# Kernel tuning notes

Hardware: AMD Instinct MI355X
Metric: run time of the kernel (lower is better)

## Reference

```python
import jax, jax.numpy as jnp
import numpy as np

# LoFTR coarse matching at 640x480 / 8 resolution
N, C = 2, 256
H0, W0, H1, W1 = 60, 80, 60, 80
L, S = H0 * W0, H1 * W1
THR = 0.2          # config['thr']
BORDER = 2         # config['border_rm']
TEMP = 0.1         # config['dsmax_temperature']


def setup_inputs() -> dict:
    key = jax.random.key(0)
    k0, k1 = jax.random.split(key)
    return {
        "feat_c0": jax.random.normal(k0, (N, L, C), dtype=jnp.float32),
        "feat_c1": jax.random.normal(k1, (N, S, C), dtype=jnp.float32),
    }


def _border_ok():
    # interior mask (no 'mask0' in data path): zero out BORDER cells on every side
    def interior(n):
        i = jnp.arange(n)
        return (i >= BORDER) & (i < n - BORDER)
    ok = (interior(H0)[:, None, None, None]
          & interior(W0)[None, :, None, None]
          & interior(H1)[None, None, :, None]
          & interior(W1)[None, None, None, :])  # [H0,W0,H1,W1]
    return ok.reshape(L, S)


def reference(feat_c0, feat_c1):
    # feature normalization by sqrt(C)
    scale = 1.0 / (C ** 0.5)
    f0 = feat_c0 * scale
    f1 = feat_c1 * scale
    # similarity + dual softmax
    sim = jnp.einsum('nlc,nsc->nls', f0, f1) / TEMP           # [N,L,S]
    conf = jax.nn.softmax(sim, axis=1) * jax.nn.softmax(sim, axis=2)
    # threshold + border removal
    mask = (conf > THR) & _border_ok()[None]                  # [N,L,S]
    # mutual nearest neighbour
    mask = mask & (conf == conf.max(axis=2, keepdims=True)) \
                & (conf == conf.max(axis=1, keepdims=True))
    # dense fixed-shape match extraction (equivalent to b_ids/i_ids/j_ids/mconf):
    mask_v = mask.any(axis=2)                                  # [N,L] row has a match
    j_ids = jnp.argmax(mask, axis=2).astype(jnp.int32)         # [N,L] matched column
    mconf = jnp.where(
        mask_v,
        jnp.take_along_axis(conf, j_ids[..., None].astype(jnp.int64), axis=2)[..., 0],
        0.0,
    )                                                          # [N,L]
    return conf, mask_v, j_ids, mconf
```

## Files before the change

kernel.cpp:

```cpp
#include <hip/hip_runtime.h>

#define L 4800
#define S 4800
#define C 256
#define NB 2
#define STRIPS 600
#define THRV 0.2f

typedef _Float16 f16;
typedef _Float16 f16x8 __attribute__((ext_vector_type(8)));
typedef float f32x4 __attribute__((ext_vector_type(4)));

__global__ __launch_bounds__(256) void k_convert(const float* __restrict__ a, const float* __restrict__ b,
                                                 f16* __restrict__ ah, f16* __restrict__ bh) {
    const int PER = NB * L * C / 4;
    int idx = blockIdx.x * 256 + threadIdx.x;
    const float4* src;
    unsigned long long* dst;
    int i;
    if (idx < PER) { src = reinterpret_cast<const float4*>(a); dst = reinterpret_cast<unsigned long long*>(ah); i = idx; }
    else           { src = reinterpret_cast<const float4*>(b); dst = reinterpret_cast<unsigned long long*>(bh); i = idx - PER; }
    float4 v = src[i];
    union { f16 h[4]; unsigned long long u; } p;
    p.h[0] = (f16)v.x; p.h[1] = (f16)v.y; p.h[2] = (f16)v.z; p.h[3] = (f16)v.w;
    dst[i] = p.u;
}

__global__ __launch_bounds__(256) void k_gemm(const f16* __restrict__ f0h, const f16* __restrict__ f1h,
                                              float* __restrict__ sim) {
    __shared__ __align__(16) unsigned char lds[65536];
    const int bi = blockIdx.x, bj = blockIdx.y, n = blockIdx.z;
    const int tid = threadIdx.x;

    const uint4* gA = reinterpret_cast<const uint4*>(f0h + ((size_t)n * L + (size_t)bi * 64) * C);
    const uint4* gB = reinterpret_cast<const uint4*>(f1h + ((size_t)n * S + (size_t)bj * 64) * C);
#pragma unroll
    for (int q = 0; q < 8; ++q) {
        int chunk = tid + 256 * q;
        int r = chunk >> 5;
        int bcol = (chunk & 31) << 4;
        int sw = bcol ^ ((r & 7) << 4);
        *reinterpret_cast<uint4*>(&lds[r * 512 + sw])         = gA[chunk];
        *reinterpret_cast<uint4*>(&lds[32768 + r * 512 + sw]) = gB[chunk];
    }
    __syncthreads();

    const int lane = tid & 63, wid = tid >> 6;
    const int wr = (wid >> 1) * 32, wc = (wid & 1) * 32;
    const int frow = lane & 15;
    const int fkByte = (lane >> 4) * 16;

    f32x4 acc[2][2] = {};
#pragma unroll
    for (int ks = 0; ks < 8; ++ks) {
        int kByte = ks * 64 + fkByte;
        f16x8 a[2], b[2];
#pragma unroll
        for (int mi = 0; mi < 2; ++mi) {
            int row = wr + mi * 16 + frow;
            a[mi] = *reinterpret_cast<const f16x8*>(&lds[row * 512 + (kByte ^ ((row & 7) << 4))]);
        }
#pragma unroll
        for (int ni = 0; ni < 2; ++ni) {
            int row = wc + ni * 16 + frow;
            b[ni] = *reinterpret_cast<const f16x8*>(&lds[32768 + row * 512 + (kByte ^ ((row & 7) << 4))]);
        }
#pragma unroll
        for (int mi = 0; mi < 2; ++mi)
#pragma unroll
            for (int ni = 0; ni < 2; ++ni)
                acc[mi][ni] = __builtin_amdgcn_mfma_f32_16x16x32_f16(a[mi], b[ni], acc[mi][ni], 0, 0, 0);
    }

    const float scale = 0.0390625f;
    const int crow0 = (lane >> 4) * 4;
    const int ccol = lane & 15;
#pragma unroll
    for (int mi = 0; mi < 2; ++mi)
#pragma unroll
        for (int ni = 0; ni < 2; ++ni)
#pragma unroll
            for (int reg = 0; reg < 4; ++reg) {
                int r = bi * 64 + wr + mi * 16 + crow0 + reg;
                int c = bj * 64 + wc + ni * 16 + ccol;
                sim[((size_t)n * L + r) * S + c] = acc[mi][ni][reg] * scale;
            }
}

__global__ __launch_bounds__(256) void k_stats(const float* __restrict__ sim, float* __restrict__ invRowSum,
                                               float* __restrict__ colPart) {
    const int strip = blockIdx.x, n = blockIdx.y, tid = threadIdx.x;
    const int r0 = strip * 8;
    const float4* base = reinterpret_cast<const float4*>(sim + ((size_t)n * L + r0) * S);
    float4* cp = reinterpret_cast<float4*>(colPart + ((size_t)n * STRIPS + strip) * S);
    float rowPart[8] = {0, 0, 0, 0, 0, 0, 0, 0};
    for (int c = tid; c < S / 4; c += 256) {
        float4 cs = {0.f, 0.f, 0.f, 0.f};
#pragma unroll
        for (int r = 0; r < 8; ++r) {
            float4 v = base[(size_t)r * (S / 4) + c];
            float e0 = __expf(v.x), e1 = __expf(v.y), e2 = __expf(v.z), e3 = __expf(v.w);
            cs.x += e0; cs.y += e1; cs.z += e2; cs.w += e3;
            rowPart[r] += (e0 + e1) + (e2 + e3);
        }
        cp[c] = cs;
    }
    __shared__ float red[4][8];
    const int lane = tid & 63, wid = tid >> 6;
#pragma unroll
    for (int r = 0; r < 8; ++r) {
        float v = rowPart[r];
#pragma unroll
        for (int o = 1; o < 64; o <<= 1) v += __shfl_xor(v, o);
        if (lane == 0) red[wid][r] = v;
    }
    __syncthreads();
    if (tid < 8) {
        float s = (red[0][tid] + red[1][tid]) + (red[2][tid] + red[3][tid]);
        invRowSum[(size_t)n * L + r0 + tid] = 1.0f / s;
    }
}

__global__ __launch_bounds__(256) void k_colreduce_a(const float* __restrict__ part, float* __restrict__ part2) {
    int j = blockIdx.x * 256 + threadIdx.x;
    int n = blockIdx.y, z = blockIdx.z;
    if (j >= S) return;
    const float* p = part + ((size_t)n * STRIPS + (size_t)z * 60) * S + j;
    float s0 = 0, s1 = 0, s2 = 0, s3 = 0;
#pragma unroll
    for (int k = 0; k < 60; k += 4) {
        s0 += p[(size_t)(k + 0) * S];
        s1 += p[(size_t)(k + 1) * S];
        s2 += p[(size_t)(k + 2) * S];
        s3 += p[(size_t)(k + 3) * S];
    }
    part2[((size_t)n * 10 + z) * S + j] = (s0 + s1) + (s2 + s3);
}
__global__ __launch_bounds__(256) void k_colreduce_b(const float* __restrict__ part2, float* __restrict__ invColSum) {
    int idx = blockIdx.x * 256 + threadIdx.x;
    if (idx >= NB * S) return;
    int n = idx / S, j = idx % S;
    const float* p = part2 + (size_t)n * 10 * S + j;
    float s = 0;
#pragma unroll
    for (int z = 0; z < 10; ++z) s += p[(size_t)z * S];
    invColSum[idx] = 1.0f / s;
}

__global__ __launch_bounds__(256) void k_conf(float* __restrict__ sim, const float* __restrict__ invRowSum,
                                              const float* __restrict__ invColSum,
                                              float* __restrict__ rowConfVal, int* __restrict__ rowConfArg,
                                              float* __restrict__ colPart) {
    const int strip = blockIdx.x, n = blockIdx.y, tid = threadIdx.x;
    const int r0 = strip * 8;
    float4* base = reinterpret_cast<float4*>(sim + ((size_t)n * L + r0) * S);
    const float4* ics = reinterpret_cast<const float4*>(invColSum + (size_t)n * S);
    float4* cp = reinterpret_cast<float4*>(colPart + ((size_t)n * STRIPS + strip) * S);
    float irs[8];
#pragma unroll
    for (int r = 0; r < 8; ++r) irs[r] = invRowSum[(size_t)n * L + r0 + r];
    float bestV[8]; int bestJ[8];
#pragma unroll
    for (int r = 0; r < 8; ++r) { bestV[r] = -1.0f; bestJ[r] = 0; }

    for (int c = tid; c < S / 4; c += 256) {
        float4 ic = ics[c];
        float4 cm = {0.f, 0.f, 0.f, 0.f};
#pragma unroll
        for (int r = 0; r < 8; ++r) {
            float4 v = base[(size_t)r * (S / 4) + c];
            float e0 = __expf(v.x), e1 = __expf(v.y), e2 = __expf(v.z), e3 = __expf(v.w);
            float c0 = e0 * e0 * irs[r] * ic.x;
            float c1 = e1 * e1 * irs[r] * ic.y;
            float c2 = e2 * e2 * irs[r] * ic.z;
            float c3 = e3 * e3 * irs[r] * ic.w;
            float4 cf; cf.x = c0; cf.y = c1; cf.z = c2; cf.w = c3;
            base[(size_t)r * (S / 4) + c] = cf;
            cm.x = fmaxf(cm.x, c0); cm.y = fmaxf(cm.y, c1); cm.z = fmaxf(cm.z, c2); cm.w = fmaxf(cm.w, c3);
            if (c0 > bestV[r]) { bestV[r] = c0; bestJ[r] = c * 4 + 0; }
            if (c1 > bestV[r]) { bestV[r] = c1; bestJ[r] = c * 4 + 1; }
            if (c2 > bestV[r]) { bestV[r] = c2; bestJ[r] = c * 4 + 2; }
            if (c3 > bestV[r]) { bestV[r] = c3; bestJ[r] = c * 4 + 3; }
        }
        cp[c] = cm;
    }
    __shared__ float rv[4][8]; __shared__ int rj[4][8];
    const int lane = tid & 63, wid = tid >> 6;
#pragma unroll
    for (int r = 0; r < 8; ++r) {
        float v = bestV[r]; int j = bestJ[r];
#pragma unroll
        for (int o = 1; o < 64; o <<= 1) {
            float ov = __shfl_xor(v, o); int oj = __shfl_xor(j, o);
            if (ov > v || (ov == v && oj < j)) { v = ov; j = oj; }
        }
        if (lane == 0) { rv[wid][r] = v; rj[wid][r] = j; }
    }
    __syncthreads();
    if (tid < 8) {
        float v = rv[0][tid]; int j = rj[0][tid];
#pragma unroll
        for (int w = 1; w < 4; ++w) {
            float ov = rv[w][tid]; int oj = rj[w][tid];
            if (ov > v || (ov == v && oj < j)) { v = ov; j = oj; }
        }
        rowConfVal[(size_t)n * L + r0 + tid] = v;
        rowConfArg[(size_t)n * L + r0 + tid] = j;
    }
}

__global__ __launch_bounds__(256) void k_colmax_a(const float* __restrict__ part, float* __restrict__ part2) {
    int j = blockIdx.x * 256 + threadIdx.x;
    int n = blockIdx.y, z = blockIdx.z;
    if (j >= S) return;
    const float* p = part + ((size_t)n * STRIPS + (size_t)z * 60) * S + j;
    float m0 = 0, m1 = 0, m2 = 0, m3 = 0;
#pragma unroll
    for (int k = 0; k < 60; k += 4) {
        m0 = fmaxf(m0, p[(size_t)(k + 0) * S]);
        m1 = fmaxf(m1, p[(size_t)(k + 1) * S]);
        m2 = fmaxf(m2, p[(size_t)(k + 2) * S]);
        m3 = fmaxf(m3, p[(size_t)(k + 3) * S]);
    }
    part2[((size_t)n * 10 + z) * S + j] = fmaxf(fmaxf(m0, m1), fmaxf(m2, m3));
}
__global__ __launch_bounds__(256) void k_colmax_b(const float* __restrict__ part2, float* __restrict__ colConfMax) {
    int idx = blockIdx.x * 256 + threadIdx.x;
    if (idx >= NB * S) return;
    int n = idx / S, j = idx % S;
    const float* p = part2 + (size_t)n * 10 * S + j;
    float m = 0;
#pragma unroll
    for (int z = 0; z < 10; ++z) m = fmaxf(m, p[(size_t)z * S]);
    colConfMax[idx] = m;
}

__global__ __launch_bounds__(256) void k_final(const float* __restrict__ rowConfVal, const int* __restrict__ rowConfArg,
                                               const float* __restrict__ colConfMax,
                                               float* __restrict__ out_maskv, float* __restrict__ out_jids,
                                               float* __restrict__ out_mconf) {
    int idx = blockIdx.x * 256 + threadIdx.x;
    if (idx >= NB * L) return;
    int n = idx / L, i = idx % L;
    float v = rowConfVal[idx];
    int j = rowConfArg[idx];
    int h0 = i / 80, w0 = i % 80;
    int h1 = j / 80, w1 = j % 80;
    bool ok = (v > THRV)
              && (h0 >= 2) && (h0 < 58) && (w0 >= 2) && (w0 < 78)
              && (h1 >= 2) && (h1 < 58) && (w1 >= 2) && (w1 < 78)
              && (v == colConfMax[(size_t)n * S + j]);
    out_maskv[idx] = ok ? 1.0f : 0.0f;
    out_jids[idx]  = ok ? (float)j : 0.0f;
    out_mconf[idx] = ok ? v : 0.0f;
}

extern "C" void kernel_launch(void* const* d_in, const int* in_sizes, int n_in,
                              void* d_out, int out_size, void* d_ws, size_t ws_size,
                              hipStream_t stream) {
    const float* f0 = (const float*)d_in[0];
    const float* f1 = (const float*)d_in[1];
    float* out = (float*)d_out;
    char* ws = (char*)d_ws;

    f16*   f0h        = (f16*)(ws + 0);
    f16*   f1h        = (f16*)(ws + 4915200);
    float* colPart    = (float*)(ws + 9830400);
    float* part2      = (float*)(ws + 32870400);
    float* invColSum  = (float*)(ws + 33254400);
    float* invRowSum  = (float*)(ws + 33292800);
    float* rowConfVal = (float*)(ws + 33331200);
    int*   rowConfArg = (int*)  (ws + 33369600);
    float* colConfMax = (float*)(ws + 33408000);

    float* sim = out;
    float* out_maskv = out + (size_t)NB * L * S;
    float* out_jids  = out_maskv + NB * L;
    float* out_mconf = out_jids + NB * L;

    k_convert<<<4800, 256, 0, stream>>>(f0, f1, f0h, f1h);
    k_gemm<<<dim3(75, 75, NB), 256, 0, stream>>>(f0h, f1h, sim);
    k_stats<<<dim3(STRIPS, NB), 256, 0, stream>>>(sim, invRowSum, colPart);
    k_colreduce_a<<<dim3(19, NB, 10), 256, 0, stream>>>(colPart, part2);
    k_colreduce_b<<<(NB * S + 255) / 256, 256, 0, stream>>>(part2, invColSum);
    k_conf<<<dim3(STRIPS, NB), 256, 0, stream>>>(sim, invRowSum, invColSum, rowConfVal, rowConfArg, colPart);
    k_colmax_a<<<dim3(19, NB, 10), 256, 0, stream>>>(colPart, part2);
    k_colmax_b<<<(NB * S + 255) / 256, 256, 0, stream>>>(part2, colConfMax);
    k_final<<<(NB * L + 255) / 256, 256, 0, stream>>>(rowConfVal, rowConfArg, colConfMax,
                                                      out_maskv, out_jids, out_mconf);
}
```

Baseline: 336.6 us.

## Recompute similarity GEMM in two fused passes instead of materializing sim

Replaces the standalone GEMM plus two full sweeps over the stored fp32 similarity matrix with two fused kernels. Each recomputes the f16 MFMA GEMM per 32-row strip and 1600-column chunk, then applies exp, row/column partial sums or conf, and max/argmax in registers. Only the final conf matrix is written, so the sim write and two 184MB reads are removed at the cost of doing the GEMM twice. B tiles are double-buffered into LDS with global_load_lds, and row results are merged across the three column chunks in extra small kernels.

```diff
diff --git a/kernel.cpp b/kernel.cpp
--- a/kernel.cpp
+++ b/kernel.cpp
@@ -4,12 +4,24 @@
 #define S 4800
 #define C 256
 #define NB 2
-#define STRIPS 600
 #define THRV 0.2f
+#define SCALE 0.0390625f
+#define NSTRIP 150
+#define NCC 3
+#define CCW 1600
+#define NT 64
+#define NTILES 25
 
 typedef _Float16 f16;
 typedef _Float16 f16x8 __attribute__((ext_vector_type(8)));
 typedef float f32x4 __attribute__((ext_vector_type(4)));
+
+typedef __attribute__((address_space(1))) const unsigned int g_as1;
+typedef __attribute__((address_space(3))) unsigned int lds_as3;
+
+__device__ __forceinline__ void gload_lds16(const void* g, void* l) {
+    __builtin_amdgcn_global_load_lds((g_as1*)g, (lds_as3*)l, 16, 0, 0);
+}
 
 __global__ __launch_bounds__(256) void k_convert(const float* __restrict__ a, const float* __restrict__ b,
                                                  f16* __restrict__ ah, f16* __restrict__ bh) {
@@ -26,186 +38,272 @@
     dst[i] = p.u;
 }
 
-__global__ __launch_bounds__(256) void k_gemm(const f16* __restrict__ f0h, const f16* __restrict__ f1h,
-                                              float* __restrict__ sim) {
-    __shared__ __align__(16) unsigned char lds[65536];
-    const int bi = blockIdx.x, bj = blockIdx.y, n = blockIdx.z;
-    const int tid = threadIdx.x;
-
-    const uint4* gA = reinterpret_cast<const uint4*>(f0h + ((size_t)n * L + (size_t)bi * 64) * C);
-    const uint4* gB = reinterpret_cast<const uint4*>(f1h + ((size_t)n * S + (size_t)bj * 64) * C);
-#pragma unroll
-    for (int q = 0; q < 8; ++q) {
-        int chunk = tid + 256 * q;
-        int r = chunk >> 5;
-        int bcol = (chunk & 31) << 4;
-        int sw = bcol ^ ((r & 7) << 4);
-        *reinterpret_cast<uint4*>(&lds[r * 512 + sw])         = gA[chunk];
-        *reinterpret_cast<uint4*>(&lds[32768 + r * 512 + sw]) = gB[chunk];
-    }
+__global__ __launch_bounds__(256) void k_pass1(const f16* __restrict__ f0h, const f16* __restrict__ f1h,
+                                               float* __restrict__ rowSumPart, float* __restrict__ colPart) {
+    __shared__ __align__(16) unsigned char lds[81920];
+    const int strip = blockIdx.x, cc = blockIdx.y, n = blockIdx.z;
+    const int tid = threadIdx.x, lane = tid & 63, w = tid >> 6;
+    const int fr = lane & 15, kg = lane >> 4;
+    const int jbase = cc * CCW;
+
+    {
+        const uint4* gA = reinterpret_cast<const uint4*>(f0h + ((size_t)n * L + strip * 32) * C);
+        uint4* As = reinterpret_cast<uint4*>(lds + 65536);
+#pragma unroll
+        for (int q = 0; q < 4; ++q) {
+            int c = tid + 256 * q;
+            int r = c >> 5, bcol = c & 31;
+            As[r * 32 + (bcol ^ (r & 7))] = gA[c];
+        }
+    }
+    const f16* gBbase = f1h + ((size_t)n * S + jbase) * C;
+    {
+        const uint4* gBt = reinterpret_cast<const uint4*>(gBbase);
+#pragma unroll
+        for (int i = 0; i < 8; ++i) {
+            int q = (w * 8 + i) * 64 + lane;
+            int r = q >> 5, bcol = q & 31;
+            gload_lds16(gBt + r * 32 + (bcol ^ (r & 7)), lds + (w * 8 + i) * 1024);
+        }
+    }
+    asm volatile("s_waitcnt vmcnt(0)" ::: "memory");
     __syncthreads();
 
-    const int lane = tid & 63, wid = tid >> 6;
-    const int wr = (wid >> 1) * 32, wc = (wid & 1) * 32;
-    const int frow = lane & 15;
-    const int fkByte = (lane >> 4) * 16;
-
-    f32x4 acc[2][2] = {};
-#pragma unroll
-    for (int ks = 0; ks < 8; ++ks) {
-        int kByte = ks * 64 + fkByte;
-        f16x8 a[2], b[2];
-#pragma unroll
-        for (int mi = 0; mi < 2; ++mi) {
-            int row = wr + mi * 16 + frow;
-            a[mi] = *reinterpret_cast<const f16x8*>(&lds[row * 512 + (kByte ^ ((row & 7) << 4))]);
-        }
-#pragma unroll
-        for (int ni = 0; ni < 2; ++ni) {
-            int row = wc + ni * 16 + frow;
-            b[ni] = *reinterpret_cast<const f16x8*>(&lds[32768 + row * 512 + (kByte ^ ((row & 7) << 4))]);
-        }
-#pragma unroll
-        for (int mi = 0; mi < 2; ++mi)
-#pragma unroll
-            for (int ni = 0; ni < 2; ++ni)
-                acc[mi][ni] = __builtin_amdgcn_mfma_f32_16x16x32_f16(a[mi], b[ni], acc[mi][ni], 0, 0, 0);
-    }
-
-    const float scale = 0.0390625f;
-    const int crow0 = (lane >> 4) * 4;
-    const int ccol = lane & 15;
+    f16x8 a[2][8];
 #pragma unroll
     for (int mi = 0; mi < 2; ++mi)
 #pragma unroll
-        for (int ni = 0; ni < 2; ++ni)
-#pragma unroll
-            for (int reg = 0; reg < 4; ++reg) {
-                int r = bi * 64 + wr + mi * 16 + crow0 + reg;
-                int c = bj * 64 + wc + ni * 16 + ccol;
-                sim[((size_t)n * L + r) * S + c] = acc[mi][ni][reg] * scale;
+        for (int ks = 0; ks < 8; ++ks) {
+            int row = mi * 16 + fr;
+            a[mi][ks] = *reinterpret_cast<const f16x8*>(lds + 65536 + (row * 32 + ((ks * 4 + kg) ^ (row & 7))) * 16);
+        }
+
+    float rowAcc[8] = {0,0,0,0,0,0,0,0};
+    const int rowb = w * 16 + fr;
+
+    for (int t = 0; t < NTILES; ++t) {
+        const int cur = t & 1;
+        if (t < NTILES - 1) {
+            const uint4* gBt = reinterpret_cast<const uint4*>(gBbase + (size_t)(t + 1) * NT * C);
+            unsigned char* dst = lds + (cur ^ 1) * 32768;
+#pragma unroll
+            for (int i = 0; i < 8; ++i) {
+                int q = (w * 8 + i) * 64 + lane;
+                int r = q >> 5, bcol = q & 31;
+                gload_lds16(gBt + r * 32 + (bcol ^ (r & 7)), dst + (w * 8 + i) * 1024);
             }
-}
-
-__global__ __launch_bounds__(256) void k_stats(const float* __restrict__ sim, float* __restrict__ invRowSum,
-                                               float* __restrict__ colPart) {
-    const int strip = blockIdx.x, n = blockIdx.y, tid = threadIdx.x;
-    const int r0 = strip * 8;
-    const float4* base = reinterpret_cast<const float4*>(sim + ((size_t)n * L + r0) * S);
-    float4* cp = reinterpret_cast<float4*>(colPart + ((size_t)n * STRIPS + strip) * S);
-    float rowPart[8] = {0, 0, 0, 0, 0, 0, 0, 0};
-    for (int c = tid; c < S / 4; c += 256) {
-        float4 cs = {0.f, 0.f, 0.f, 0.f};
-#pragma unroll
-        for (int r = 0; r < 8; ++r) {
-            float4 v = base[(size_t)r * (S / 4) + c];
-            float e0 = __expf(v.x), e1 = __expf(v.y), e2 = __expf(v.z), e3 = __expf(v.w);
-            cs.x += e0; cs.y += e1; cs.z += e2; cs.w += e3;
-            rowPart[r] += (e0 + e1) + (e2 + e3);
-        }
-        cp[c] = cs;
-    }
-    __shared__ float red[4][8];
-    const int lane = tid & 63, wid = tid >> 6;
-#pragma unroll
-    for (int r = 0; r < 8; ++r) {
-        float v = rowPart[r];
-#pragma unroll
-        for (int o = 1; o < 64; o <<= 1) v += __shfl_xor(v, o);
-        if (lane == 0) red[wid][r] = v;
+            asm volatile("s_waitcnt vmcnt(8)" ::: "memory");
+        } else {
+            asm volatile("s_waitcnt vmcnt(0)" ::: "memory");
+        }
+        __builtin_amdgcn_s_barrier();
+        asm volatile("" ::: "memory");
+
+        const unsigned char* Bb = lds + cur * 32768;
+        f32x4 acc0 = {0.f,0.f,0.f,0.f}, acc1 = {0.f,0.f,0.f,0.f};
+#pragma unroll
+        for (int ks = 0; ks < 8; ++ks) {
+            f16x8 bf = *reinterpret_cast<const f16x8*>(Bb + (rowb * 32 + ((ks * 4 + kg) ^ (rowb & 7))) * 16);
+            acc0 = __builtin_amdgcn_mfma_f32_16x16x32_f16(a[0][ks], bf, acc0, 0, 0, 0);
+            acc1 = __builtin_amdgcn_mfma_f32_16x16x32_f16(a[1][ks], bf, acc1, 0, 0, 0);
+        }
+        float colv = 0.f;
+#pragma unroll
+        for (int r4 = 0; r4 < 4; ++r4) {
+            float e0 = __expf(acc0[r4] * SCALE); rowAcc[r4] += e0;
+            float e1 = __expf(acc1[r4] * SCALE); rowAcc[4 + r4] += e1;
+            colv += e0 + e1;
+        }
+        colv += __shfl_xor(colv, 16); colv += __shfl_xor(colv, 32);
+        if (lane < 16)
+            colPart[((size_t)n * NSTRIP + strip) * S + jbase + t * NT + w * 16 + lane] = colv;
+        asm volatile("" ::: "memory");
+        __builtin_amdgcn_s_barrier();
+    }
+
+#pragma unroll
+    for (int o = 1; o < 16; o <<= 1)
+#pragma unroll
+        for (int r8 = 0; r8 < 8; ++r8) rowAcc[r8] += __shfl_xor(rowAcc[r8], o);
+    float* scratch = reinterpret_cast<float*>(lds + 65536);
+    if ((lane & 15) == 0) {
+#pragma unroll
+        for (int r8 = 0; r8 < 8; ++r8) {
+            int row = (r8 >> 2) * 16 + kg * 4 + (r8 & 3);
+            scratch[w * 32 + row] = rowAcc[r8];
+        }
     }
     __syncthreads();
-    if (tid < 8) {
-        float s = (red[0][tid] + red[1][tid]) + (red[2][tid] + red[3][tid]);
-        invRowSum[(size_t)n * L + r0 + tid] = 1.0f / s;
-    }
+    if (tid < 32)
+        rowSumPart[((size_t)n * NCC + cc) * L + strip * 32 + tid] =
+            (scratch[tid] + scratch[32 + tid]) + (scratch[64 + tid] + scratch[96 + tid]);
+}
+
+__global__ __launch_bounds__(256) void k_rowinv(const float* __restrict__ rowSumPart, float* __restrict__ invRowSum) {
+    int idx = blockIdx.x * 256 + threadIdx.x;
+    if (idx >= NB * L) return;
+    int n = idx / L, row = idx % L;
+    float s = rowSumPart[((size_t)n * NCC + 0) * L + row]
+            + rowSumPart[((size_t)n * NCC + 1) * L + row]
+            + rowSumPart[((size_t)n * NCC + 2) * L + row];
+    invRowSum[idx] = 1.0f / s;
 }
 
 __global__ __launch_bounds__(256) void k_colreduce_a(const float* __restrict__ part, float* __restrict__ part2) {
     int j = blockIdx.x * 256 + threadIdx.x;
     int n = blockIdx.y, z = blockIdx.z;
     if (j >= S) return;
-    const float* p = part + ((size_t)n * STRIPS + (size_t)z * 60) * S + j;
-    float s0 = 0, s1 = 0, s2 = 0, s3 = 0;
-#pragma unroll
-    for (int k = 0; k < 60; k += 4) {
-        s0 += p[(size_t)(k + 0) * S];
-        s1 += p[(size_t)(k + 1) * S];
-        s2 += p[(size_t)(k + 2) * S];
-        s3 += p[(size_t)(k + 3) * S];
-    }
-    part2[((size_t)n * 10 + z) * S + j] = (s0 + s1) + (s2 + s3);
+    const float* p = part + ((size_t)n * NSTRIP + (size_t)z * 15) * S + j;
+    float s = 0.f;
+#pragma unroll
+    for (int k = 0; k < 15; ++k) s += p[(size_t)k * S];
+    part2[((size_t)n * 10 + z) * S + j] = s;
 }
 __global__ __launch_bounds__(256) void k_colreduce_b(const float* __restrict__ part2, float* __restrict__ invColSum) {
     int idx = blockIdx.x * 256 + threadIdx.x;
     if (idx >= NB * S) return;
     int n = idx / S, j = idx % S;
     const float* p = part2 + (size_t)n * 10 * S + j;
-    float s = 0;
+    float s = 0.f;
 #pragma unroll
     for (int z = 0; z < 10; ++z) s += p[(size_t)z * S];
     invColSum[idx] = 1.0f / s;
 }
 
-__global__ __launch_bounds__(256) void k_conf(float* __restrict__ sim, const float* __restrict__ invRowSum,
-                                              const float* __restrict__ invColSum,
-                                              float* __restrict__ rowConfVal, int* __restrict__ rowConfArg,
-                                              float* __restrict__ colPart) {
-    const int strip = blockIdx.x, n = blockIdx.y, tid = threadIdx.x;
-    const int r0 = strip * 8;
-    float4* base = reinterpret_cast<float4*>(sim + ((size_t)n * L + r0) * S);
-    const float4* ics = reinterpret_cast<const float4*>(invColSum + (size_t)n * S);
-    float4* cp = reinterpret_cast<float4*>(colPart + ((size_t)n * STRIPS + strip) * S);
+__global__ __launch_bounds__(256) void k_pass2(const f16* __restrict__ f0h, const f16* __restrict__ f1h,
+                                               const float* __restrict__ invRowSum, const float* __restrict__ invColSum,
+                                               float* __restrict__ conf,
+                                               float* __restrict__ rowValPart, int* __restrict__ rowArgPart,
+                                               float* __restrict__ colPart) {
+    __shared__ __align__(16) unsigned char lds[81920];
+    const int strip = blockIdx.x, cc = blockIdx.y, n = blockIdx.z;
+    const int tid = threadIdx.x, lane = tid & 63, w = tid >> 6;
+    const int fr = lane & 15, kg = lane >> 4;
+    const int jbase = cc * CCW;
+
+    {
+        const uint4* gA = reinterpret_cast<const uint4*>(f0h + ((size_t)n * L + strip * 32) * C);
+        uint4* As = reinterpret_cast<uint4*>(lds + 65536);
+#pragma unroll
+        for (int q = 0; q < 4; ++q) {
+            int c = tid + 256 * q;
+            int r = c >> 5, bcol = c & 31;
+            As[r * 32 + (bcol ^ (r & 7))] = gA[c];
+        }
+    }
+    const f16* gBbase = f1h + ((size_t)n * S + jbase) * C;
+    {
+        const uint4* gBt = reinterpret_cast<const uint4*>(gBbase);
+#pragma unroll
+        for (int i = 0; i < 8; ++i) {
+            int q = (w * 8 + i) * 64 + lane;
+            int r = q >> 5, bcol = q & 31;
+            gload_lds16(gBt + r * 32 + (bcol ^ (r & 7)), lds + (w * 8 + i) * 1024);
+        }
+    }
+    asm volatile("s_waitcnt vmcnt(0)" ::: "memory");
+    __syncthreads();
+
+    f16x8 a[2][8];
+#pragma unroll
+    for (int mi = 0; mi < 2; ++mi)
+#pragma unroll
+        for (int ks = 0; ks < 8; ++ks) {
+            int row = mi * 16 + fr;
+            a[mi][ks] = *reinterpret_cast<const f16x8*>(lds + 65536 + (row * 32 + ((ks * 4 + kg) ^ (row & 7))) * 16);
+        }
+
     float irs[8];
 #pragma unroll
-    for (int r = 0; r < 8; ++r) irs[r] = invRowSum[(size_t)n * L + r0 + r];
+    for (int r8 = 0; r8 < 8; ++r8)
+        irs[r8] = invRowSum[(size_t)n * L + strip * 32 + (r8 >> 2) * 16 + kg * 4 + (r8 & 3)];
+
     float bestV[8]; int bestJ[8];
 #pragma unroll
-    for (int r = 0; r < 8; ++r) { bestV[r] = -1.0f; bestJ[r] = 0; }
-
-    for (int c = tid; c < S / 4; c += 256) {
-        float4 ic = ics[c];
-        float4 cm = {0.f, 0.f, 0.f, 0.f};
-#pragma unroll
-        for (int r = 0; r < 8; ++r) {
-            float4 v = base[(size_t)r * (S / 4) + c];
-            float e0 = __expf(v.x), e1 = __expf(v.y), e2 = __expf(v.z), e3 = __expf(v.w);
-            float c0 = e0 * e0 * irs[r] * ic.x;
-            float c1 = e1 * e1 * irs[r] * ic.y;
-            float c2 = e2 * e2 * irs[r] * ic.z;
-            float c3 = e3 * e3 * irs[r] * ic.w;
-            float4 cf; cf.x = c0; cf.y = c1; cf.z = c2; cf.w = c3;
-            base[(size_t)r * (S / 4) + c] = cf;
-            cm.x = fmaxf(cm.x, c0); cm.y = fmaxf(cm.y, c1); cm.z = fmaxf(cm.z, c2); cm.w = fmaxf(cm.w, c3);
-            if (c0 > bestV[r]) { bestV[r] = c0; bestJ[r] = c * 4 + 0; }
-            if (c1 > bestV[r]) { bestV[r] = c1; bestJ[r] = c * 4 + 1; }
-            if (c2 > bestV[r]) { bestV[r] = c2; bestJ[r] = c * 4 + 2; }
-            if (c3 > bestV[r]) { bestV[r] = c3; bestJ[r] = c * 4 + 3; }
-        }
-        cp[c] = cm;
-    }
-    __shared__ float rv[4][8]; __shared__ int rj[4][8];
-    const int lane = tid & 63, wid = tid >> 6;
-#pragma unroll
-    for (int r = 0; r < 8; ++r) {
-        float v = bestV[r]; int j = bestJ[r];
-#pragma unroll
-        for (int o = 1; o < 64; o <<= 1) {
-            float ov = __shfl_xor(v, o); int oj = __shfl_xor(j, o);
+    for (int r8 = 0; r8 < 8; ++r8) { bestV[r8] = -1.0f; bestJ[r8] = 0; }
+
+    const int rowb = w * 16 + fr;
+    float* crowBase = conf + ((size_t)n * L + strip * 32) * S + jbase + w * 16 + fr;
+
+    for (int t = 0; t < NTILES; ++t) {
+        const int cur = t & 1;
+        if (t < NTILES - 1) {
+            const uint4* gBt = reinterpret_cast<const uint4*>(gBbase + (size_t)(t + 1) * NT * C);
+            unsigned char* dst = lds + (cur ^ 1) * 32768;
+#pragma unroll
+            for (int i = 0; i < 8; ++i) {
+                int q = (w * 8 + i) * 64 + lane;
+                int r = q >> 5, bcol = q & 31;
+                gload_lds16(gBt + r * 32 + (bcol ^ (r & 7)), dst + (w * 8 + i) * 1024);
+            }
+            asm volatile("s_waitcnt vmcnt(8)" ::: "memory");
+        } else {
+            asm volatile("s_waitcnt vmcnt(0)" ::: "memory");
+        }
+        __builtin_amdgcn_s_barrier();
+        asm volatile("" ::: "memory");
+
+        const unsigned char* Bb = lds + cur * 32768;
+        f32x4 acc0 = {0.f,0.f,0.f,0.f}, acc1 = {0.f,0.f,0.f,0.f};
+#pragma unroll
+        for (int ks = 0; ks < 8; ++ks) {
+            f16x8 bf = *reinterpret_cast<const f16x8*>(Bb + (rowb * 32 + ((ks * 4 + kg) ^ (rowb & 7))) * 16);
+            acc0 = __builtin_amdgcn_mfma_f32_16x16x32_f16(a[0][ks], bf, acc0, 0, 0, 0);
+            acc1 = __builtin_amdgcn_mfma_f32_16x16x32_f16(a[1][ks], bf, acc1, 0, 0, 0);
+        }
+
+        const int jcol = jbase + t * NT + w * 16 + fr;
+        float icol = invColSum[(size_t)n * S + jcol];
+        float* crow = crowBase + t * NT;
+        float cmax = 0.f;
+#pragma unroll
+        for (int r4 = 0; r4 < 4; ++r4) {
+            float e0 = __expf(acc0[r4] * SCALE);
+            float cf0 = e0 * e0 * irs[r4] * icol;
+            crow[(size_t)(kg * 4 + r4) * S] = cf0;
+            if (cf0 > bestV[r4]) { bestV[r4] = cf0; bestJ[r4] = jcol; }
+            float e1 = __expf(acc1[r4] * SCALE);
+            float cf1 = e1 * e1 * irs[4 + r4] * icol;
+            crow[(size_t)(16 + kg * 4 + r4) * S] = cf1;
+            if (cf1 > bestV[4 + r4]) { bestV[4 + r4] = cf1; bestJ[4 + r4] = jcol; }
+            cmax = fmaxf(cmax, fmaxf(cf0, cf1));
+        }
+        cmax = fmaxf(cmax, __shfl_xor(cmax, 16));
+        cmax = fmaxf(cmax, __shfl_xor(cmax, 32));
+        if (lane < 16)
+            colPart[((size_t)n * NSTRIP + strip) * S + jcol] = cmax;
+        asm volatile("" ::: "memory");
+        __builtin_amdgcn_s_barrier();
+    }
+
+#pragma unroll
+    for (int o = 1; o < 16; o <<= 1)
+#pragma unroll
+        for (int r8 = 0; r8 < 8; ++r8) {
+            float ov = __shfl_xor(bestV[r8], o);
+            int oj = __shfl_xor(bestJ[r8], o);
+            if (ov > bestV[r8] || (ov == bestV[r8] && oj < bestJ[r8])) { bestV[r8] = ov; bestJ[r8] = oj; }
+        }
+    float* sv = reinterpret_cast<float*>(lds + 65536);
+    int* sj = reinterpret_cast<int*>(lds + 65536 + 512);
+    if ((lane & 15) == 0) {
+#pragma unroll
+        for (int r8 = 0; r8 < 8; ++r8) {
+            int row = (r8 >> 2) * 16 + kg * 4 + (r8 & 3);
+            sv[w * 32 + row] = bestV[r8];
+            sj[w * 32 + row] = bestJ[r8];
+        }
+    }
+    __syncthreads();
+    if (tid < 32) {
+        float v = sv[tid]; int j = sj[tid];
+#pragma unroll
+        for (int w2 = 1; w2 < 4; ++w2) {
+            float ov = sv[w2 * 32 + tid]; int oj = sj[w2 * 32 + tid];
             if (ov > v || (ov == v && oj < j)) { v = ov; j = oj; }
         }
-        if (lane == 0) { rv[wid][r] = v; rj[wid][r] = j; }
-    }
-    __syncthreads();
-    if (tid < 8) {
-        float v = rv[0][tid]; int j = rj[0][tid];
-#pragma unroll
-        for (int w = 1; w < 4; ++w) {
-            float ov = rv[w][tid]; int oj = rj[w][tid];
-            if (ov > v || (ov == v && oj < j)) { v = ov; j = oj; }
-        }
-        rowConfVal[(size_t)n * L + r0 + tid] = v;
-        rowConfArg[(size_t)n * L + r0 + tid] = j;
+        rowValPart[((size_t)n * NCC + cc) * L + strip * 32 + tid] = v;
+        rowArgPart[((size_t)n * NCC + cc) * L + strip * 32 + tid] = j;
     }
 }
 
@@ -213,37 +311,38 @@
     int j = blockIdx.x * 256 + threadIdx.x;
     int n = blockIdx.y, z = blockIdx.z;
     if (j >= S) return;
-    const float* p = part + ((size_t)n * STRIPS + (size_t)z * 60) * S + j;
-    float m0 = 0, m1 = 0, m2 = 0, m3 = 0;
-#pragma unroll
-    for (int k = 0; k < 60; k += 4) {
-        m0 = fmaxf(m0, p[(size_t)(k + 0) * S]);
-        m1 = fmaxf(m1, p[(size_t)(k + 1) * S]);
-        m2 = fmaxf(m2, p[(size_t)(k + 2) * S]);
-        m3 = fmaxf(m3, p[(size_t)(k + 3) * S]);
-    }
-    part2[((size_t)n * 10 + z) * S + j] = fmaxf(fmaxf(m0, m1), fmaxf(m2, m3));
+    const float* p = part + ((size_t)n * NSTRIP + (size_t)z * 15) * S + j;
+    float m = 0.f;
+#pragma unroll
+    for (int k = 0; k < 15; ++k) m = fmaxf(m, p[(size_t)k * S]);
+    part2[((size_t)n * 10 + z) * S + j] = m;
 }
 __global__ __launch_bounds__(256) void k_colmax_b(const float* __restrict__ part2, float* __restrict__ colConfMax) {
     int idx = blockIdx.x * 256 + threadIdx.x;
     if (idx >= NB * S) return;
     int n = idx / S, j = idx % S;
     const float* p = part2 + (size_t)n * 10 * S + j;
-    float m = 0;
+    float m = 0.f;
 #pragma unroll
     for (int z = 0; z < 10; ++z) m = fmaxf(m, p[(size_t)z * S]);
     colConfMax[idx] = m;
 }
 
-__global__ __launch_bounds__(256) void k_final(const float* __restrict__ rowConfVal, const int* __restrict__ rowConfArg,
+__global__ __launch_bounds__(256) void k_final(const float* __restrict__ rowValPart, const int* __restrict__ rowArgPart,
                                                const float* __restrict__ colConfMax,
                                                float* __restrict__ out_maskv, float* __restrict__ out_jids,
                                                float* __restrict__ out_mconf) {
     int idx = blockIdx.x * 256 + threadIdx.x;
     if (idx >= NB * L) return;
     int n = idx / L, i = idx % L;
-    float v = rowConfVal[idx];
-    int j = rowConfArg[idx];
+    float v = rowValPart[((size_t)n * NCC + 0) * L + i];
+    int j = rowArgPart[((size_t)n * NCC + 0) * L + i];
+#pragma unroll
+    for (int cc = 1; cc < NCC; ++cc) {
+        float ov = rowValPart[((size_t)n * NCC + cc) * L + i];
+        int oj = rowArgPart[((size_t)n * NCC + cc) * L + i];
+        if (ov > v || (ov == v && oj < j)) { v = ov; j = oj; }
+    }
     int h0 = i / 80, w0 = i % 80;
     int h1 = j / 80, w1 = j % 80;
     bool ok = (v > THRV)
@@ -266,26 +365,28 @@
     f16*   f0h        = (f16*)(ws + 0);
     f16*   f1h        = (f16*)(ws + 4915200);
     float* colPart    = (float*)(ws + 9830400);
-    float* part2      = (float*)(ws + 32870400);
-    float* invColSum  = (float*)(ws + 33254400);
-    float* invRowSum  = (float*)(ws + 33292800);
-    float* rowConfVal = (float*)(ws + 33331200);
-    int*   rowConfArg = (int*)  (ws + 33369600);
-    float* colConfMax = (float*)(ws + 33408000);
-
-    float* sim = out;
+    float* part2      = (float*)(ws + 15590400);
+    float* rowSumPart = (float*)(ws + 15974400);
+    float* rowValPart = (float*)(ws + 16089600);
+    int*   rowArgPart = (int*)  (ws + 16204800);
+    float* invRowSum  = (float*)(ws + 16320000);
+    float* invColSum  = (float*)(ws + 16358400);
+    float* colConfMax = (float*)(ws + 16396800);
+
+    float* conf = out;
     float* out_maskv = out + (size_t)NB * L * S;
     float* out_jids  = out_maskv + NB * L;
     float* out_mconf = out_jids + NB * L;
 
     k_convert<<<4800, 256, 0, stream>>>(f0, f1, f0h, f1h);
-    k_gemm<<<dim3(75, 75, NB), 256, 0, stream>>>(f0h, f1h, sim);
-    k_stats<<<dim3(STRIPS, NB), 256, 0, stream>>>(sim, invRowSum, colPart);
+    k_pass1<<<dim3(NSTRIP, NCC, NB), 256, 0, stream>>>(f0h, f1h, rowSumPart, colPart);
+    k_rowinv<<<(NB * L + 255) / 256, 256, 0, stream>>>(rowSumPart, invRowSum);
     k_colreduce_a<<<dim3(19, NB, 10), 256, 0, stream>>>(colPart, part2);
     k_colreduce_b<<<(NB * S + 255) / 256, 256, 0, stream>>>(part2, invColSum);
-    k_conf<<<dim3(STRIPS, NB), 256, 0, stream>>>(sim, invRowSum, invColSum, rowConfVal, rowConfArg, colPart);
+    k_pass2<<<dim3(NSTRIP, NCC, NB), 256, 0, stream>>>(f0h, f1h, invRowSum, invColSum, conf,
+                                                       rowValPart, rowArgPart, colPart);
     k_colmax_a<<<dim3(19, NB, 10), 256, 0, stream>>>(colPart, part2);
     k_colmax_b<<<(NB * S + 255) / 256, 256, 0, stream>>>(part2, colConfMax);
-    k_final<<<(NB * L + 255) / 256, 256, 0, stream>>>(rowConfVal, rowConfArg, colConfMax,
+    k_final<<<(NB * L + 255) / 256, 256, 0, stream>>>(rowValPart, rowArgPart, colConfMax,
                                                       out_maskv, out_jids, out_mconf);
 }
```

New measurement: 305.2 us. -9.3%, faster.

## Fuse GEMM with exp and row/col sums, store exp as fp16, two-pass conf

Applied to the files above, without the earlier changes.

The similarity GEMM now computes exp(sim) directly in its epilogue. It accumulates row sums in registers and column sums through atomics, and writes exp values as an fp16 intermediate instead of fp32 sim. A second pass reads the fp16 exp values and forms conf as e^2 scaled by the inverse row and column sums. That pass does the row argmax and an atomic column max, which replaces the separate stats, colreduce and colmax kernels and cuts full-matrix traffic. The GEMM keeps A fragments in registers and double-buffers B tiles with direct global-to-LDS loads. Storing exp in fp16 loses precision and could overflow for large similarities, and the atomics make the sums order-nondeterministic.

```diff
diff --git a/kernel.cpp b/kernel.cpp
--- a/kernel.cpp
+++ b/kernel.cpp
@@ -4,12 +4,26 @@
 #define S 4800
 #define C 256
 #define NB 2
-#define STRIPS 600
 #define THRV 0.2f
+#define SCALE 0.0390625f
+#define NST1 75
+#define NCC 3
+#define CCW 1600
+#define NT 64
+#define NTILES 25
+#define P2R 20
+#define NST2 240
 
 typedef _Float16 f16;
 typedef _Float16 f16x8 __attribute__((ext_vector_type(8)));
 typedef float f32x4 __attribute__((ext_vector_type(4)));
+
+typedef __attribute__((address_space(1))) const unsigned int g_as1;
+typedef __attribute__((address_space(3))) unsigned int lds_as3;
+
+__device__ __forceinline__ void gload_lds16(const void* g, void* l) {
+    __builtin_amdgcn_global_load_lds((g_as1*)g, (lds_as3*)l, 16, 0, 0);
+}
 
 __global__ __launch_bounds__(256) void k_convert(const float* __restrict__ a, const float* __restrict__ b,
                                                  f16* __restrict__ ah, f16* __restrict__ bh) {
@@ -26,230 +40,194 @@
     dst[i] = p.u;
 }
 
-__global__ __launch_bounds__(256) void k_gemm(const f16* __restrict__ f0h, const f16* __restrict__ f1h,
-                                              float* __restrict__ sim) {
+__global__ __launch_bounds__(256) void k_pass1(const f16* __restrict__ f0h, const f16* __restrict__ f1h,
+                                               f16* __restrict__ E, float* __restrict__ rowSum,
+                                               float* __restrict__ colSum) {
     __shared__ __align__(16) unsigned char lds[65536];
-    const int bi = blockIdx.x, bj = blockIdx.y, n = blockIdx.z;
+    const int strip = blockIdx.x, cc = blockIdx.y, n = blockIdx.z;
+    const int tid = threadIdx.x, lane = tid & 63, w = tid >> 6;
+    const int fr = lane & 15, kg = lane >> 4;
+    const int jbase = cc * CCW;
+
+    const f16* gBbase = f1h + ((size_t)n * S + jbase) * C;
+    {
+        const uint4* gBt = reinterpret_cast<const uint4*>(gBbase);
+#pragma unroll
+        for (int i = 0; i < 8; ++i) {
+            int q = (w * 8 + i) * 64 + lane;
+            int r = q >> 5, bcol = q & 31;
+            gload_lds16(gBt + r * 32 + (bcol ^ (r & 7)), lds + (w * 8 + i) * 1024);
+        }
+    }
+    f16x8 a[4][8];
+    const f16* Ab = f0h + ((size_t)n * L + strip * 64) * C;
+#pragma unroll
+    for (int mi = 0; mi < 4; ++mi)
+#pragma unroll
+        for (int ks = 0; ks < 8; ++ks)
+            a[mi][ks] = *reinterpret_cast<const f16x8*>(Ab + (mi * 16 + fr) * C + ks * 32 + kg * 8);
+
+    asm volatile("s_waitcnt vmcnt(0)" ::: "memory");
+    __syncthreads();
+
+    float rowAcc[16] = {};
+    const int rowb = w * 16 + fr;
+    f16* Ebase = E + ((size_t)n * L + strip * 64 + kg * 4) * S + jbase + w * 16 + fr;
+
+    for (int t = 0; t < NTILES; ++t) {
+        const int cur = t & 1;
+        if (t < NTILES - 1) {
+            const uint4* gBt = reinterpret_cast<const uint4*>(gBbase + (size_t)(t + 1) * NT * C);
+            unsigned char* dst = lds + (cur ^ 1) * 32768;
+#pragma unroll
+            for (int i = 0; i < 8; ++i) {
+                int q = (w * 8 + i) * 64 + lane;
+                int r = q >> 5, bcol = q & 31;
+                gload_lds16(gBt + r * 32 + (bcol ^ (r & 7)), dst + (w * 8 + i) * 1024);
+            }
+            asm volatile("s_waitcnt vmcnt(25)" ::: "memory");
+        } else {
+            asm volatile("s_waitcnt vmcnt(17)" ::: "memory");
+        }
+        __builtin_amdgcn_s_barrier();
+        asm volatile("" ::: "memory");
+
+        const unsigned char* Bb = lds + cur * 32768;
+        f32x4 acc[4] = {};
+#pragma unroll
+        for (int ks = 0; ks < 8; ++ks) {
+            f16x8 bf = *reinterpret_cast<const f16x8*>(Bb + (rowb * 32 + ((ks * 4 + kg) ^ (rowb & 7))) * 16);
+#pragma unroll
+            for (int mi = 0; mi < 4; ++mi)
+                acc[mi] = __builtin_amdgcn_mfma_f32_16x16x32_f16(a[mi][ks], bf, acc[mi], 0, 0, 0);
+        }
+
+        float colv = 0.f;
+        f16* ep = Ebase + t * NT;
+#pragma unroll
+        for (int mi = 0; mi < 4; ++mi)
+#pragma unroll
+            for (int r4 = 0; r4 < 4; ++r4) {
+                float ef = __expf(acc[mi][r4] * SCALE);
+                rowAcc[mi * 4 + r4] += ef;
+                colv += ef;
+                ep[(size_t)(mi * 16 + r4) * S] = (f16)ef;
+            }
+        colv += __shfl_xor(colv, 16);
+        colv += __shfl_xor(colv, 32);
+        if (lane < 16)
+            unsafeAtomicAdd(&colSum[(size_t)n * S + jbase + t * NT + w * 16 + lane], colv);
+        asm volatile("" ::: "memory");
+        __builtin_amdgcn_s_barrier();
+    }
+
+#pragma unroll
+    for (int o = 1; o < 16; o <<= 1)
+#pragma unroll
+        for (int i = 0; i < 16; ++i) rowAcc[i] += __shfl_xor(rowAcc[i], o);
+    if (fr == 0) {
+#pragma unroll
+        for (int mi = 0; mi < 4; ++mi)
+#pragma unroll
+            for (int r4 = 0; r4 < 4; ++r4)
+                unsafeAtomicAdd(&rowSum[(size_t)n * L + strip * 64 + mi * 16 + kg * 4 + r4],
+                                rowAcc[mi * 4 + r4]);
+    }
+}
+
+__global__ __launch_bounds__(256) void k_pass2(const f16* __restrict__ E,
+                                               const float* __restrict__ rowSum, const float* __restrict__ colSum,
+                                               float* __restrict__ conf,
+                                               float* __restrict__ rowVal, int* __restrict__ rowArg,
+                                               int* __restrict__ colMaxI) {
+    __shared__ float icsL[S];
+    __shared__ float irsL[P2R];
+    __shared__ float rvL[4][P2R];
+    __shared__ int rjL[4][P2R];
+    const int strip = blockIdx.x, n = blockIdx.y;
+    const int r0 = strip * P2R;
     const int tid = threadIdx.x;
-
-    const uint4* gA = reinterpret_cast<const uint4*>(f0h + ((size_t)n * L + (size_t)bi * 64) * C);
-    const uint4* gB = reinterpret_cast<const uint4*>(f1h + ((size_t)n * S + (size_t)bj * 64) * C);
-#pragma unroll
-    for (int q = 0; q < 8; ++q) {
-        int chunk = tid + 256 * q;
-        int r = chunk >> 5;
-        int bcol = (chunk & 31) << 4;
-        int sw = bcol ^ ((r & 7) << 4);
-        *reinterpret_cast<uint4*>(&lds[r * 512 + sw])         = gA[chunk];
-        *reinterpret_cast<uint4*>(&lds[32768 + r * 512 + sw]) = gB[chunk];
-    }
+    for (int c = tid; c < S; c += 256) icsL[c] = 1.0f / colSum[(size_t)n * S + c];
+    if (tid < P2R) irsL[tid] = 1.0f / rowSum[(size_t)n * L + r0 + tid];
     __syncthreads();
 
-    const int lane = tid & 63, wid = tid >> 6;
-    const int wr = (wid >> 1) * 32, wc = (wid & 1) * 32;
-    const int frow = lane & 15;
-    const int fkByte = (lane >> 4) * 16;
-
-    f32x4 acc[2][2] = {};
-#pragma unroll
-    for (int ks = 0; ks < 8; ++ks) {
-        int kByte = ks * 64 + fkByte;
-        f16x8 a[2], b[2];
-#pragma unroll
-        for (int mi = 0; mi < 2; ++mi) {
-            int row = wr + mi * 16 + frow;
-            a[mi] = *reinterpret_cast<const f16x8*>(&lds[row * 512 + (kByte ^ ((row & 7) << 4))]);
-        }
-#pragma unroll
-        for (int ni = 0; ni < 2; ++ni) {
-            int row = wc + ni * 16 + frow;
-            b[ni] = *reinterpret_cast<const f16x8*>(&lds[32768 + row * 512 + (kByte ^ ((row & 7) << 4))]);
-        }
-#pragma unroll
-        for (int mi = 0; mi < 2; ++mi)
-#pragma unroll
-            for (int ni = 0; ni < 2; ++ni)
-                acc[mi][ni] = __builtin_amdgcn_mfma_f32_16x16x32_f16(a[mi], b[ni], acc[mi][ni], 0, 0, 0);
-    }
-
-    const float scale = 0.0390625f;
-    const int crow0 = (lane >> 4) * 4;
-    const int ccol = lane & 15;
-#pragma unroll
-    for (int mi = 0; mi < 2; ++mi)
-#pragma unroll
-        for (int ni = 0; ni < 2; ++ni)
-#pragma unroll
-            for (int reg = 0; reg < 4; ++reg) {
-                int r = bi * 64 + wr + mi * 16 + crow0 + reg;
-                int c = bj * 64 + wc + ni * 16 + ccol;
-                sim[((size_t)n * L + r) * S + c] = acc[mi][ni][reg] * scale;
+    float bestV[P2R]; int bestJ[P2R];
+#pragma unroll
+    for (int r = 0; r < P2R; ++r) { bestV[r] = -1.0f; bestJ[r] = 0; }
+
+    const f16* Eb = E + ((size_t)n * L + r0) * S;
+    float* Cb = conf + ((size_t)n * L + r0) * S;
+
+    for (int c = tid; c < S / 8; c += 256) {
+        const int j0 = c * 8;
+        float ics[8];
+#pragma unroll
+        for (int k = 0; k < 8; ++k) ics[k] = icsL[j0 + k];
+        float colm[8];
+#pragma unroll
+        for (int k = 0; k < 8; ++k) colm[k] = 0.f;
+#pragma unroll
+        for (int r = 0; r < P2R; ++r) {
+            f16x8 ev = *reinterpret_cast<const f16x8*>(Eb + (size_t)r * S + j0);
+            const float irs = irsL[r];
+            float cf[8];
+#pragma unroll
+            for (int k = 0; k < 8; ++k) {
+                float e = (float)ev[k];
+                cf[k] = (e * e * irs) * ics[k];
+                colm[k] = fmaxf(colm[k], cf[k]);
+                if (cf[k] > bestV[r]) { bestV[r] = cf[k]; bestJ[r] = j0 + k; }
             }
-}
-
-__global__ __launch_bounds__(256) void k_stats(const float* __restrict__ sim, float* __restrict__ invRowSum,
-                                               float* __restrict__ colPart) {
-    const int strip = blockIdx.x, n = blockIdx.y, tid = threadIdx.x;
-    const int r0 = strip * 8;
-    const float4* base = reinterpret_cast<const float4*>(sim + ((size_t)n * L + r0) * S);
-    float4* cp = reinterpret_cast<float4*>(colPart + ((size_t)n * STRIPS + strip) * S);
-    float rowPart[8] = {0, 0, 0, 0, 0, 0, 0, 0};
-    for (int c = tid; c < S / 4; c += 256) {
-        float4 cs = {0.f, 0.f, 0.f, 0.f};
-#pragma unroll
-        for (int r = 0; r < 8; ++r) {
-            float4 v = base[(size_t)r * (S / 4) + c];
-            float e0 = __expf(v.x), e1 = __expf(v.y), e2 = __expf(v.z), e3 = __expf(v.w);
-            cs.x += e0; cs.y += e1; cs.z += e2; cs.w += e3;
-            rowPart[r] += (e0 + e1) + (e2 + e3);
-        }
-        cp[c] = cs;
-    }
-    __shared__ float red[4][8];
-    const int lane = tid & 63, wid = tid >> 6;
-#pragma unroll
-    for (int r = 0; r < 8; ++r) {
-        float v = rowPart[r];
-#pragma unroll
-        for (int o = 1; o < 64; o <<= 1) v += __shfl_xor(v, o);
-        if (lane == 0) red[wid][r] = v;
-    }
-    __syncthreads();
-    if (tid < 8) {
-        float s = (red[0][tid] + red[1][tid]) + (red[2][tid] + red[3][tid]);
-        invRowSum[(size_t)n * L + r0 + tid] = 1.0f / s;
-    }
-}
-
-__global__ __launch_bounds__(256) void k_colreduce_a(const float* __restrict__ part, float* __restrict__ part2) {
-    int j = blockIdx.x * 256 + threadIdx.x;
-    int n = blockIdx.y, z = blockIdx.z;
-    if (j >= S) return;
-    const float* p = part + ((size_t)n * STRIPS + (size_t)z * 60) * S + j;
-    float s0 = 0, s1 = 0, s2 = 0, s3 = 0;
-#pragma unroll
-    for (int k = 0; k < 60; k += 4) {
-        s0 += p[(size_t)(k + 0) * S];
-        s1 += p[(size_t)(k + 1) * S];
-        s2 += p[(size_t)(k + 2) * S];
-        s3 += p[(size_t)(k + 3) * S];
-    }
-    part2[((size_t)n * 10 + z) * S + j] = (s0 + s1) + (s2 + s3);
-}
-__global__ __launch_bounds__(256) void k_colreduce_b(const float* __restrict__ part2, float* __restrict__ invColSum) {
-    int idx = blockIdx.x * 256 + threadIdx.x;
-    if (idx >= NB * S) return;
-    int n = idx / S, j = idx % S;
-    const float* p = part2 + (size_t)n * 10 * S + j;
-    float s = 0;
-#pragma unroll
-    for (int z = 0; z < 10; ++z) s += p[(size_t)z * S];
-    invColSum[idx] = 1.0f / s;
-}
-
-__global__ __launch_bounds__(256) void k_conf(float* __restrict__ sim, const float* __restrict__ invRowSum,
-                                              const float* __restrict__ invColSum,
-                                              float* __restrict__ rowConfVal, int* __restrict__ rowConfArg,
-                                              float* __restrict__ colPart) {
-    const int strip = blockIdx.x, n = blockIdx.y, tid = threadIdx.x;
-    const int r0 = strip * 8;
-    float4* base = reinterpret_cast<float4*>(sim + ((size_t)n * L + r0) * S);
-    const float4* ics = reinterpret_cast<const float4*>(invColSum + (size_t)n * S);
-    float4* cp = reinterpret_cast<float4*>(colPart + ((size_t)n * STRIPS + strip) * S);
-    float irs[8];
-#pragma unroll
-    for (int r = 0; r < 8; ++r) irs[r] = invRowSum[(size_t)n * L + r0 + r];
-    float bestV[8]; int bestJ[8];
-#pragma unroll
-    for (int r = 0; r < 8; ++r) { bestV[r] = -1.0f; bestJ[r] = 0; }
-
-    for (int c = tid; c < S / 4; c += 256) {
-        float4 ic = ics[c];
-        float4 cm = {0.f, 0.f, 0.f, 0.f};
-#pragma unroll
-        for (int r = 0; r < 8; ++r) {
-            float4 v = base[(size_t)r * (S / 4) + c];
-            float e0 = __expf(v.x), e1 = __expf(v.y), e2 = __expf(v.z), e3 = __expf(v.w);
-            float c0 = e0 * e0 * irs[r] * ic.x;
-            float c1 = e1 * e1 * irs[r] * ic.y;
-            float c2 = e2 * e2 * irs[r] * ic.z;
-            float c3 = e3 * e3 * irs[r] * ic.w;
-            float4 cf; cf.x = c0; cf.y = c1; cf.z = c2; cf.w = c3;
-            base[(size_t)r * (S / 4) + c] = cf;
-            cm.x = fmaxf(cm.x, c0); cm.y = fmaxf(cm.y, c1); cm.z = fmaxf(cm.z, c2); cm.w = fmaxf(cm.w, c3);
-            if (c0 > bestV[r]) { bestV[r] = c0; bestJ[r] = c * 4 + 0; }
-            if (c1 > bestV[r]) { bestV[r] = c1; bestJ[r] = c * 4 + 1; }
-            if (c2 > bestV[r]) { bestV[r] = c2; bestJ[r] = c * 4 + 2; }
-            if (c3 > bestV[r]) { bestV[r] = c3; bestJ[r] = c * 4 + 3; }
-        }
-        cp[c] = cm;
-    }
-    __shared__ float rv[4][8]; __shared__ int rj[4][8];
-    const int lane = tid & 63, wid = tid >> 6;
-#pragma unroll
-    for (int r = 0; r < 8; ++r) {
+            float4 w0 = {cf[0], cf[1], cf[2], cf[3]};
+            float4 w1 = {cf[4], cf[5], cf[6], cf[7]};
+            float4* cp = reinterpret_cast<float4*>(Cb + (size_t)r * S + j0);
+            cp[0] = w0; cp[1] = w1;
+        }
+#pragma unroll
+        for (int k = 0; k < 8; ++k)
+            atomicMax(&colMaxI[(size_t)n * S + j0 + k], __float_as_int(colm[k]));
+    }
+
+    const int lane = tid & 63, wv = tid >> 6;
+#pragma unroll
+    for (int r = 0; r < P2R; ++r) {
         float v = bestV[r]; int j = bestJ[r];
 #pragma unroll
         for (int o = 1; o < 64; o <<= 1) {
             float ov = __shfl_xor(v, o); int oj = __shfl_xor(j, o);
             if (ov > v || (ov == v && oj < j)) { v = ov; j = oj; }
         }
-        if (lane == 0) { rv[wid][r] = v; rj[wid][r] = j; }
+        if (lane == 0) { rvL[wv][r] = v; rjL[wv][r] = j; }
     }
     __syncthreads();
-    if (tid < 8) {
-        float v = rv[0][tid]; int j = rj[0][tid];
-#pragma unroll
-        for (int w = 1; w < 4; ++w) {
-            float ov = rv[w][tid]; int oj = rj[w][tid];
+    if (tid < P2R) {
+        float v = rvL[0][tid]; int j = rjL[0][tid];
+#pragma unroll
+        for (int q = 1; q < 4; ++q) {
+            float ov = rvL[q][tid]; int oj = rjL[q][tid];
             if (ov > v || (ov == v && oj < j)) { v = ov; j = oj; }
         }
-        rowConfVal[(size_t)n * L + r0 + tid] = v;
-        rowConfArg[(size_t)n * L + r0 + tid] = j;
-    }
-}
-
-__global__ __launch_bounds__(256) void k_colmax_a(const float* __restrict__ part, float* __restrict__ part2) {
-    int j = blockIdx.x * 256 + threadIdx.x;
-    int n = blockIdx.y, z = blockIdx.z;
-    if (j >= S) return;
-    const float* p = part + ((size_t)n * STRIPS + (size_t)z * 60) * S + j;
-    float m0 = 0, m1 = 0, m2 = 0, m3 = 0;
-#pragma unroll
-    for (int k = 0; k < 60; k += 4) {
-        m0 = fmaxf(m0, p[(size_t)(k + 0) * S]);
-        m1 = fmaxf(m1, p[(size_t)(k + 1) * S]);
-        m2 = fmaxf(m2, p[(size_t)(k + 2) * S]);
-        m3 = fmaxf(m3, p[(size_t)(k + 3) * S]);
-    }
-    part2[((size_t)n * 10 + z) * S + j] = fmaxf(fmaxf(m0, m1), fmaxf(m2, m3));
-}
-__global__ __launch_bounds__(256) void k_colmax_b(const float* __restrict__ part2, float* __restrict__ colConfMax) {
-    int idx = blockIdx.x * 256 + threadIdx.x;
-    if (idx >= NB * S) return;
-    int n = idx / S, j = idx % S;
-    const float* p = part2 + (size_t)n * 10 * S + j;
-    float m = 0;
-#pragma unroll
-    for (int z = 0; z < 10; ++z) m = fmaxf(m, p[(size_t)z * S]);
-    colConfMax[idx] = m;
-}
-
-__global__ __launch_bounds__(256) void k_final(const float* __restrict__ rowConfVal, const int* __restrict__ rowConfArg,
-                                               const float* __restrict__ colConfMax,
+        rowVal[(size_t)n * L + r0 + tid] = v;
+        rowArg[(size_t)n * L + r0 + tid] = j;
+    }
+}
+
+__global__ __launch_bounds__(256) void k_final(const float* __restrict__ rowVal, const int* __restrict__ rowArg,
+                                               const int* __restrict__ colMaxI,
                                                float* __restrict__ out_maskv, float* __restrict__ out_jids,
                                                float* __restrict__ out_mconf) {
     int idx = blockIdx.x * 256 + threadIdx.x;
     if (idx >= NB * L) return;
     int n = idx / L, i = idx % L;
-    float v = rowConfVal[idx];
-    int j = rowConfArg[idx];
+    float v = rowVal[idx];
+    int j = rowArg[idx];
+    float cm = __int_as_float(colMaxI[(size_t)n * S + j]);
     int h0 = i / 80, w0 = i % 80;
     int h1 = j / 80, w1 = j % 80;
     bool ok = (v > THRV)
               && (h0 >= 2) && (h0 < 58) && (w0 >= 2) && (w0 < 78)
               && (h1 >= 2) && (h1 < 58) && (w1 >= 2) && (w1 < 78)
-              && (v == colConfMax[(size_t)n * S + j]);
+              && (v == cm);
     out_maskv[idx] = ok ? 1.0f : 0.0f;
     out_jids[idx]  = ok ? (float)j : 0.0f;
     out_mconf[idx] = ok ? v : 0.0f;
@@ -263,29 +241,24 @@
     float* out = (float*)d_out;
     char* ws = (char*)d_ws;
 
-    f16*   f0h        = (f16*)(ws + 0);
-    f16*   f1h        = (f16*)(ws + 4915200);
-    float* colPart    = (float*)(ws + 9830400);
-    float* part2      = (float*)(ws + 32870400);
-    float* invColSum  = (float*)(ws + 33254400);
-    float* invRowSum  = (float*)(ws + 33292800);
-    float* rowConfVal = (float*)(ws + 33331200);
-    int*   rowConfArg = (int*)  (ws + 33369600);
-    float* colConfMax = (float*)(ws + 33408000);
-
-    float* sim = out;
+    f16*   f0h     = (f16*)(ws + 0);
+    f16*   f1h     = (f16*)(ws + 4915200);
+    f16*   E       = (f16*)(ws + 9830400);
+    float* rowSum  = (float*)(ws + 101990400);
+    float* colSum  = (float*)(ws + 102028800);
+    int*   colMaxI = (int*)  (ws + 102067200);
+    float* rowVal  = (float*)(ws + 102105600);
+    int*   rowArg  = (int*)  (ws + 102144000);
+
+    float* conf = out;
     float* out_maskv = out + (size_t)NB * L * S;
     float* out_jids  = out_maskv + NB * L;
     float* out_mconf = out_jids + NB * L;
 
+    hipMemsetAsync(ws + 101990400, 0, 115200, stream);
     k_convert<<<4800, 256, 0, stream>>>(f0, f1, f0h, f1h);
-    k_gemm<<<dim3(75, 75, NB), 256, 0, stream>>>(f0h, f1h, sim);
-    k_stats<<<dim3(STRIPS, NB), 256, 0, stream>>>(sim, invRowSum, colPart);
-    k_colreduce_a<<<dim3(19, NB, 10), 256, 0, stream>>>(colPart, part2);
-    k_colreduce_b<<<(NB * S + 255) / 256, 256, 0, stream>>>(part2, invColSum);
-    k_conf<<<dim3(STRIPS, NB), 256, 0, stream>>>(sim, invRowSum, invColSum, rowConfVal, rowConfArg, colPart);
-    k_colmax_a<<<dim3(19, NB, 10), 256, 0, stream>>>(colPart, part2);
-    k_colmax_b<<<(NB * S + 255) / 256, 256, 0, stream>>>(part2, colConfMax);
-    k_final<<<(NB * L + 255) / 256, 256, 0, stream>>>(rowConfVal, rowConfArg, colConfMax,
+    k_pass1<<<dim3(NST1, NCC, NB), 256, 0, stream>>>(f0h, f1h, E, rowSum, colSum);
+    k_pass2<<<dim3(NST2, NB), 256, 0, stream>>>(E, rowSum, colSum, conf, rowVal, rowArg, colMaxI);
+    k_final<<<(NB * L + 255) / 256, 256, 0, stream>>>(rowVal, rowArg, colMaxI,
                                                       out_maskv, out_jids, out_mconf);
 }
```

Result: slower. 383.1 us (+13.8%).
